# Kernel tuning notes

Hardware: AMD Instinct MI355X
Metric: run time of the kernel (lower is better)

The kernel has to match this reference:

```python
import jax, jax.numpy as jnp
import numpy as np

EPS_LN = 1e-5


def segment_softmax(logits, seg, num_segments):
    m = jax.ops.segment_max(logits, seg, num_segments=num_segments)
    e = jnp.exp(logits - m[seg])
    s = jax.ops.segment_sum(e, seg, num_segments=num_segments)
    return e / (s[seg] + 1e-16)


def transformer_conv(x, src, dst, edge_attr, Wq, bq, Wk, bk, Wv, bv, We, Ws, bs):
    # PyG TransformerConv, heads=1: key/value gathered at source, query at dst,
    # transformed edge feature added to both key and value (message).
    N, D = x.shape[0], Wq.shape[1]
    q = (x @ Wq + bq)[dst]                      # [E, D]
    e = edge_attr @ We                          # [E, D] (lin_edge, no bias)
    k = (x @ Wk + bk)[src] + e                  # [E, D]
    v = (x @ Wv + bv)[src] + e                  # [E, D]
    alpha = segment_softmax((q * k).sum(-1) / jnp.sqrt(jnp.float32(D)), dst, N)
    agg = jax.ops.segment_sum(alpha[:, None] * v, dst, num_segments=N)
    return agg + x @ Ws + bs                    # root_weight skip connection


def graph_layer_norm(x, w, b):
    # PyG LayerNorm mode='graph': normalize over all nodes AND features of the graph.
    mu = x.mean()
    xc = x - mu
    var = (xc * xc).mean()
    return xc * jax.lax.rsqrt(var + EPS_LN) * w + b


def setup_inputs():
    key = jax.random.key(0)
    ks = jax.random.split(key, 32)
    N, E, F_NODE, F_EDGE, H, D_OUT = 50000, 800000, 64, 16, 128, 1
    g = lambda k, shp, s=0.05: jax.random.normal(k, shp, jnp.float32) * s
    inp = {
        'x': jax.random.normal(ks[0], (N, F_NODE), jnp.float32),
        'edge_index': jax.random.randint(ks[1], (2, E), 0, N),
        'edge_attr': jax.random.normal(ks[2], (E, F_EDGE), jnp.float32),
        'fc1_w': g(ks[3], (F_NODE, H)), 'fc1_b': jnp.zeros((H,), jnp.float32),
        'c1_Wq': g(ks[4], (H, H)), 'c1_bq': jnp.zeros((H,), jnp.float32),
        'c1_Wk': g(ks[5], (H, H)), 'c1_bk': jnp.zeros((H,), jnp.float32),
        'c1_Wv': g(ks[6], (H, H)), 'c1_bv': jnp.zeros((H,), jnp.float32),
        'c1_We': g(ks[7], (F_EDGE, H)),
        'c1_Ws': g(ks[8], (H, H)), 'c1_bs': jnp.zeros((H,), jnp.float32),
        'ln1_w': jnp.ones((H,), jnp.float32), 'ln1_b': jnp.zeros((H,), jnp.float32),
        'c2_Wq': g(ks[9], (H, H)), 'c2_bq': jnp.zeros((H,), jnp.float32),
        'c2_Wk': g(ks[10], (H, H)), 'c2_bk': jnp.zeros((H,), jnp.float32),
        'c2_Wv': g(ks[11], (H, H)), 'c2_bv': jnp.zeros((H,), jnp.float32),
        'c2_We': g(ks[12], (F_EDGE, H)),
        'c2_Ws': g(ks[13], (H, H)), 'c2_bs': jnp.zeros((H,), jnp.float32),
        'ln2_w': jnp.ones((H,), jnp.float32), 'ln2_b': jnp.zeros((H,), jnp.float32),
        'fc2_w': g(ks[14], (H, D_OUT)), 'fc2_b': jnp.zeros((D_OUT,), jnp.float32),
    }
    return inp


def reference(x, edge_index, edge_attr,
              fc1_w, fc1_b,
              c1_Wq, c1_bq, c1_Wk, c1_bk, c1_Wv, c1_bv, c1_We, c1_Ws, c1_bs,
              ln1_w, ln1_b,
              c2_Wq, c2_bq, c2_Wk, c2_bk, c2_Wv, c2_bv, c2_We, c2_Ws, c2_bs,
              ln2_w, ln2_b,
              fc2_w, fc2_b):
    src, dst = edge_index[0], edge_index[1]
    hx = x @ fc1_w + fc1_b
    h = transformer_conv(hx, src, dst, edge_attr,
                         c1_Wq, c1_bq, c1_Wk, c1_bk, c1_Wv, c1_bv, c1_We, c1_Ws, c1_bs)
    h = jax.nn.relu(graph_layer_norm(h, ln1_w, ln1_b))
    h = transformer_conv(h, src, dst, edge_attr,
                         c2_Wq, c2_bq, c2_Wk, c2_bk, c2_Wv, c2_bv, c2_We, c2_Ws, c2_bs)
    h = jax.nn.relu(graph_layer_norm(h, ln2_w, ln2_b))
    return h @ fc2_w + fc2_b
```

## Files before the change

kernel.cpp:

```cpp
#include <hip/hip_runtime.h>
#include <math.h>

#define HH 128
#define FIN 64
#define FE 16
#define SCAN_CHUNK 512

__global__ __launch_bounds__(256) void zero_int4(int4* __restrict__ p, int n4) {
  const int stride = gridDim.x * 256;
  for (int i = blockIdx.x * 256 + threadIdx.x; i < n4; i += stride)
    p[i] = make_int4(0, 0, 0, 0);
}

__global__ __launch_bounds__(256) void hist_kernel(
    const int* __restrict__ dstArr, int* __restrict__ deg, int E) {
  const int e = blockIdx.x * 256 + threadIdx.x;
  if (e < E) atomicAdd(deg + dstArr[e], 1);
}

__global__ __launch_bounds__(256) void scan1(
    const int* __restrict__ deg, int* __restrict__ out, int* __restrict__ sums, int n) {
  __shared__ int lds[256];
  const int t = threadIdx.x;
  const int i0 = blockIdx.x * SCAN_CHUNK + t * 2;
  const int v0 = (i0 < n) ? deg[i0] : 0;
  const int v1 = (i0 + 1 < n) ? deg[i0 + 1] : 0;
  const int tsum = v0 + v1;
  lds[t] = tsum;
  __syncthreads();
  for (int off = 1; off < 256; off <<= 1) {
    const int x = (t >= off) ? lds[t - off] : 0;
    __syncthreads();
    lds[t] += x;
    __syncthreads();
  }
  const int excl = lds[t] - tsum;
  if (i0 < n) out[i0] = excl;
  if (i0 + 1 < n) out[i0 + 1] = excl + v0;
  if (t == 255) sums[blockIdx.x] = lds[255];
}

__global__ __launch_bounds__(256) void scan2(int* __restrict__ sums, int nb) {
  __shared__ int lds[256];
  const int t = threadIdx.x;
  const int v = (t < nb) ? sums[t] : 0;
  lds[t] = v;
  __syncthreads();
  for (int off = 1; off < 256; off <<= 1) {
    const int x = (t >= off) ? lds[t - off] : 0;
    __syncthreads();
    lds[t] += x;
    __syncthreads();
  }
  if (t < nb) sums[t] = lds[t] - v;
}

__global__ __launch_bounds__(256) void scan3(
    int* __restrict__ out, const int* __restrict__ sums, int n) {
  const int add = sums[blockIdx.x];
  const int i0 = blockIdx.x * SCAN_CHUNK + threadIdx.x * 2;
  if (i0 < n) out[i0] += add;
  if (i0 + 1 < n) out[i0 + 1] += add;
}

__global__ __launch_bounds__(256) void scatter_kernel(
    const int* __restrict__ dstArr, const int* __restrict__ off,
    int* __restrict__ cursor, int* __restrict__ eids, int E) {
  const int e = blockIdx.x * 256 + threadIdx.x;
  if (e < E) {
    const int d = dstArr[e];
    const int p = atomicAdd(cursor + d, 1);
    eids[off[d] + p] = e;
  }
}

template<int K, int RB>
__global__ __launch_bounds__(128) void gemm_rows(
    const float* __restrict__ in, const float* __restrict__ W,
    const float* __restrict__ bias, float* __restrict__ out, int nrows) {
  __shared__ float tile[RB * K];
  const int r0 = blockIdx.x * RB;
  const int tid = threadIdx.x;
  {
    const int rows = min(RB, nrows - r0);
    const int cnt = rows * K / 4;
    const float4* src = (const float4*)(in + (size_t)r0 * K);
    float4* dst = (float4*)tile;
    for (int i = tid; i < cnt; i += 128) dst[i] = src[i];
  }
  __syncthreads();
  const int j = tid;
  float acc[RB];
  const float bj = bias[j];
#pragma unroll
  for (int r = 0; r < RB; ++r) acc[r] = bj;
#pragma unroll 4
  for (int k = 0; k < K; ++k) {
    float w = W[k * HH + j];
#pragma unroll
    for (int r = 0; r < RB; ++r) acc[r] += tile[r * K + k] * w;
  }
#pragma unroll
  for (int r = 0; r < RB; ++r) {
    int row = r0 + r;
    if (row < nrows) out[(size_t)row * HH + j] = acc[r];
  }
}

template<int RB>
__global__ __launch_bounds__(128) void qkvs_kernel(
    float* __restrict__ x,
    const float* __restrict__ Wq, const float* __restrict__ bq,
    const float* __restrict__ Wk, const float* __restrict__ bk,
    const float* __restrict__ Wv, const float* __restrict__ bv,
    const float* __restrict__ Ws, const float* __restrict__ bs,
    float* __restrict__ q, float* __restrict__ k, float* __restrict__ v,
    int nrows) {
  __shared__ float tile[RB * HH];
  const int r0 = blockIdx.x * RB;
  const int tid = threadIdx.x;
  {
    const int rows = min(RB, nrows - r0);
    const int cnt = rows * HH / 4;
    const float4* src = (const float4*)(x + (size_t)r0 * HH);
    float4* dst = (float4*)tile;
    for (int i = tid; i < cnt; i += 128) dst[i] = src[i];
  }
  __syncthreads();
  const int j = tid;
  float aq[RB], ak[RB], av[RB], as_[RB];
  const float bqj = bq[j], bkj = bk[j], bvj = bv[j], bsj = bs[j];
#pragma unroll
  for (int r = 0; r < RB; ++r) { aq[r] = bqj; ak[r] = bkj; av[r] = bvj; as_[r] = bsj; }
#pragma unroll 2
  for (int kk = 0; kk < HH; ++kk) {
    const float wq = Wq[kk * HH + j];
    const float wk = Wk[kk * HH + j];
    const float wv = Wv[kk * HH + j];
    const float ws = Ws[kk * HH + j];
#pragma unroll
    for (int r = 0; r < RB; ++r) {
      const float xv = tile[r * HH + kk];
      aq[r] += xv * wq; ak[r] += xv * wk; av[r] += xv * wv; as_[r] += xv * ws;
    }
  }
#pragma unroll
  for (int r = 0; r < RB; ++r) {
    int row = r0 + r;
    if (row < nrows) {
      const size_t o = (size_t)row * HH + j;
      q[o] = aq[r]; k[o] = ak[r]; v[o] = av[r]; x[o] = as_[r];
    }
  }
}

__global__ __launch_bounds__(256) void dst_conv(
    const int* __restrict__ csr_off, const int* __restrict__ deg,
    const int* __restrict__ csr_eid, const int* __restrict__ srcArr,
    const float* __restrict__ ea, const float* __restrict__ We,
    const float* __restrict__ q, const float* __restrict__ k,
    const float* __restrict__ v, float* __restrict__ xio,
    double* __restrict__ partials, int N) {
  const int lane = threadIdx.x & 63;
  const int wv = (blockIdx.x * blockDim.x + threadIdx.x) >> 6;
  const int nw = (gridDim.x * blockDim.x) >> 6;
  const int f0 = lane * 2;
  float wec0[FE], wec1[FE];
#pragma unroll
  for (int i = 0; i < FE; ++i) {
    wec0[i] = We[i * HH + f0];
    wec1[i] = We[i * HH + f0 + 1];
  }
  const float rs = 0.088388347648318447f;
  float s = 0.f, sq = 0.f;
  for (int d = wv; d < N; d += nw) {
    const int du = __builtin_amdgcn_readfirstlane(d);
    const int off = csr_off[du];
    const int cnt = deg[du];
    const float2 qv = *(const float2*)(q + (size_t)du * HH + f0);
    float a0 = 0.f, a1 = 0.f, wsum = 0.f;
    int eid = (cnt > 0) ? __builtin_amdgcn_readfirstlane(csr_eid[off]) : 0;
    int sn  = (cnt > 0) ? __builtin_amdgcn_readfirstlane(srcArr[eid]) : 0;
    for (int i = 0; i < cnt; ++i) {
      const int eid_n = (i + 1 < cnt) ? __builtin_amdgcn_readfirstlane(csr_eid[off + i + 1]) : 0;
      const int sn_n  = (i + 1 < cnt) ? __builtin_amdgcn_readfirstlane(srcArr[eid_n]) : 0;
      const float4* eap4 = (const float4*)(ea + (size_t)eid * FE);
      const float4 e0 = eap4[0], e1 = eap4[1], e2 = eap4[2], e3 = eap4[3];
      float ep0, ep1;
      ep0 = e0.x * wec0[0] + e0.y * wec0[1] + e0.z * wec0[2] + e0.w * wec0[3]
          + e1.x * wec0[4] + e1.y * wec0[5] + e1.z * wec0[6] + e1.w * wec0[7]
          + e2.x * wec0[8] + e2.y * wec0[9] + e2.z * wec0[10] + e2.w * wec0[11]
          + e3.x * wec0[12] + e3.y * wec0[13] + e3.z * wec0[14] + e3.w * wec0[15];
      ep1 = e0.x * wec1[0] + e0.y * wec1[1] + e0.z * wec1[2] + e0.w * wec1[3]
          + e1.x * wec1[4] + e1.y * wec1[5] + e1.z * wec1[6] + e1.w * wec1[7]
          + e2.x * wec1[8] + e2.y * wec1[9] + e2.z * wec1[10] + e2.w * wec1[11]
          + e3.x * wec1[12] + e3.y * wec1[13] + e3.z * wec1[14] + e3.w * wec1[15];
      const float2 kv = *(const float2*)(k + (size_t)sn * HH + f0);
      const float2 vv = *(const float2*)(v + (size_t)sn * HH + f0);
      float part = qv.x * (kv.x + ep0) + qv.y * (kv.y + ep1);
#pragma unroll
      for (int o = 32; o; o >>= 1) part += __shfl_xor(part, o);
      const float w = __expf(part * rs);
      wsum += w;
      a0 += w * (vv.x + ep0);
      a1 += w * (vv.y + ep1);
      eid = eid_n;
      sn = sn_n;
    }
    const float inv = 1.0f / (wsum + 1e-16f);
    float* xr = xio + (size_t)du * HH + f0;
    const float o0 = fmaf(a0, inv, xr[0]);
    const float o1 = fmaf(a1, inv, xr[1]);
    xr[0] = o0;
    xr[1] = o1;
    s += o0 + o1;
    sq += o0 * o0 + o1 * o1;
  }
#pragma unroll
  for (int o = 32; o; o >>= 1) {
    s += __shfl_xor(s, o);
    sq += __shfl_xor(sq, o);
  }
  __shared__ double red[8];
  const int w = threadIdx.x >> 6;
  if ((threadIdx.x & 63) == 0) { red[w * 2] = (double)s; red[w * 2 + 1] = (double)sq; }
  __syncthreads();
  if (threadIdx.x == 0) {
    partials[(size_t)blockIdx.x * 2] = red[0] + red[2] + red[4] + red[6];
    partials[(size_t)blockIdx.x * 2 + 1] = red[1] + red[3] + red[5] + red[7];
  }
}

__global__ __launch_bounds__(256) void ln_reduce2(
    const double* __restrict__ partials, int nb, float* __restrict__ stats,
    double inv_count) {
  double s = 0.0, sq = 0.0;
  for (int i = threadIdx.x; i < nb; i += 256) {
    s += partials[(size_t)i * 2];
    sq += partials[(size_t)i * 2 + 1];
  }
#pragma unroll
  for (int off = 32; off; off >>= 1) {
    s += __shfl_xor(s, off);
    sq += __shfl_xor(sq, off);
  }
  __shared__ double red[8];
  const int w = threadIdx.x >> 6;
  if ((threadIdx.x & 63) == 0) { red[w * 2] = s; red[w * 2 + 1] = sq; }
  __syncthreads();
  if (threadIdx.x == 0) {
    double S = 0, SQ = 0;
    for (int i = 0; i < 4; ++i) { S += red[i * 2]; SQ += red[i * 2 + 1]; }
    const double mu = S * inv_count;
    const double var = SQ * inv_count - mu * mu;
    stats[0] = (float)mu;
    stats[1] = (float)(1.0 / sqrt(var + 1e-5));
  }
}

__global__ __launch_bounds__(256) void ln_apply(
    float* __restrict__ x, const float* __restrict__ stats,
    const float* __restrict__ w, const float* __restrict__ b, int total4) {
  const int i = blockIdx.x * 256 + threadIdx.x;
  if (i >= total4) return;
  const float mu = stats[0], rstd = stats[1];
  const float4 xv = ((const float4*)x)[i];
  const float4 wv = ((const float4*)w)[i & 31];
  const float4 bv = ((const float4*)b)[i & 31];
  float4 o;
  o.x = fmaxf(fmaf((xv.x - mu) * rstd, wv.x, bv.x), 0.f);
  o.y = fmaxf(fmaf((xv.y - mu) * rstd, wv.y, bv.y), 0.f);
  o.z = fmaxf(fmaf((xv.z - mu) * rstd, wv.z, bv.z), 0.f);
  o.w = fmaxf(fmaf((xv.w - mu) * rstd, wv.w, bv.w), 0.f);
  ((float4*)x)[i] = o;
}

__global__ __launch_bounds__(256) void fc2_kernel(
    const float* __restrict__ h, const float* __restrict__ w,
    const float* __restrict__ b, float* __restrict__ out, int n) {
  const int lane = threadIdx.x & 63;
  const int node = (blockIdx.x * blockDim.x + threadIdx.x) >> 6;
  if (node >= n) return;
  const float2 hv = *(const float2*)(h + (size_t)node * HH + lane * 2);
  const float2 wv = *(const float2*)(w + lane * 2);
  float p = hv.x * wv.x + hv.y * wv.y;
#pragma unroll
  for (int off = 32; off; off >>= 1) p += __shfl_xor(p, off);
  if (lane == 0) out[node] = p + b[0];
}

extern "C" void kernel_launch(void* const* d_in, const int* in_sizes, int n_in,
                              void* d_out, int out_size, void* d_ws, size_t ws_size,
                              hipStream_t stream) {
  const float* x      = (const float*)d_in[0];
  const int*   eidx   = (const int*)d_in[1];
  const float* ea     = (const float*)d_in[2];
  const float* fc1_w  = (const float*)d_in[3];
  const float* fc1_b  = (const float*)d_in[4];
  const float* c1_Wq  = (const float*)d_in[5];
  const float* c1_bq  = (const float*)d_in[6];
  const float* c1_Wk  = (const float*)d_in[7];
  const float* c1_bk  = (const float*)d_in[8];
  const float* c1_Wv  = (const float*)d_in[9];
  const float* c1_bv  = (const float*)d_in[10];
  const float* c1_We  = (const float*)d_in[11];
  const float* c1_Ws  = (const float*)d_in[12];
  const float* c1_bs  = (const float*)d_in[13];
  const float* ln1_w  = (const float*)d_in[14];
  const float* ln1_b  = (const float*)d_in[15];
  const float* c2_Wq  = (const float*)d_in[16];
  const float* c2_bq  = (const float*)d_in[17];
  const float* c2_Wk  = (const float*)d_in[18];
  const float* c2_bk  = (const float*)d_in[19];
  const float* c2_Wv  = (const float*)d_in[20];
  const float* c2_bv  = (const float*)d_in[21];
  const float* c2_We  = (const float*)d_in[22];
  const float* c2_Ws  = (const float*)d_in[23];
  const float* c2_bs  = (const float*)d_in[24];
  const float* ln2_w  = (const float*)d_in[25];
  const float* ln2_b  = (const float*)d_in[26];
  const float* fc2_w  = (const float*)d_in[27];
  const float* fc2_b  = (const float*)d_in[28];

  const int N = in_sizes[0] / FIN;
  const int E = in_sizes[2] / FE;
  const int* srcA = eidx;
  const int* dstA = eidx + E;

  float* ws    = (float*)d_ws;
  const size_t NH = (size_t)N * HH;
  float* bufX  = ws;
  float* qb    = ws + NH;
  float* kb    = ws + 2 * NH;
  float* vb    = ws + 3 * NH;
  int* ibase   = (int*)(ws + 4 * NH);
  int* deg     = ibase;
  int* cursor  = ibase + N;
  int* csr_off = ibase + 2 * N;
  int* csr_eid = ibase + 3 * N;
  size_t icnt  = ((size_t)3 * N + E + 3) & ~(size_t)3;
  double* partials = (double*)(ibase + icnt);
  const int NB = 2048;
  float* stats = (float*)(partials + 2 * NB);
  int* sums    = (int*)(stats + 4);

  const int total4 = (int)(NH / 4);
  const int gRows  = (N + 15) / 16;
  const int gE     = (E + 255) / 256;
  const int nb1    = (N + SCAN_CHUNK - 1) / SCAN_CHUNK;
  const double invC = 1.0 / (double)NH;

  zero_int4<<<128, 256, 0, stream>>>((int4*)deg, (2 * N + 3) / 4);
  hist_kernel<<<gE, 256, 0, stream>>>(dstA, deg, E);
  scan1<<<nb1, 256, 0, stream>>>(deg, csr_off, sums, N);
  scan2<<<1, 256, 0, stream>>>(sums, nb1);
  scan3<<<nb1, 256, 0, stream>>>(csr_off, sums, N);
  scatter_kernel<<<gE, 256, 0, stream>>>(dstA, csr_off, cursor, csr_eid, E);

  gemm_rows<FIN, 16><<<gRows, 128, 0, stream>>>(x, fc1_w, fc1_b, bufX, N);
  qkvs_kernel<16><<<gRows, 128, 0, stream>>>(bufX, c1_Wq, c1_bq, c1_Wk, c1_bk,
                                             c1_Wv, c1_bv, c1_Ws, c1_bs,
                                             qb, kb, vb, N);
  dst_conv<<<NB, 256, 0, stream>>>(csr_off, deg, csr_eid, srcA, ea, c1_We,
                                   qb, kb, vb, bufX, partials, N);
  ln_reduce2<<<1, 256, 0, stream>>>(partials, NB, stats, invC);
  ln_apply<<<(total4 + 255) / 256, 256, 0, stream>>>(bufX, stats, ln1_w, ln1_b, total4);

  qkvs_kernel<16><<<gRows, 128, 0, stream>>>(bufX, c2_Wq, c2_bq, c2_Wk, c2_bk,
                                             c2_Wv, c2_bv, c2_Ws, c2_bs,
                                             qb, kb, vb, N);
  dst_conv<<<NB, 256, 0, stream>>>(csr_off, deg, csr_eid, srcA, ea, c2_We,
                                   qb, kb, vb, bufX, partials, N);
  ln_reduce2<<<1, 256, 0, stream>>>(partials, NB, stats, invC);
  ln_apply<<<(total4 + 255) / 256, 256, 0, stream>>>(bufX, stats, ln2_w, ln2_b, total4);

  fc2_kernel<<<(N + 3) / 4, 256, 0, stream>>>(bufX, fc2_w, fc2_b, (float*)d_out, N);
}
```

Before: 979.0 us.

## Factor edge projection out of per-edge loop and process nodes with 16-lane groups

Uses linearity to avoid projecting edge features to 128 dims per edge. A new kernel precomputes q·We^T (16 values per node), so the score only needs a 16-wide dot with the raw edge attributes. The weighted sum of edge attributes is accumulated per node and multiplied by We once at the end. Each destination node is now handled by a 16-lane group with float4 loads instead of a full wavefront, which cuts per-edge FLOPs and widens memory accesses. This adds a small extra kernel and workspace buffer, and trades lane parallelism per node for more nodes in flight, which may increase divergence on skewed degree distributions.

```diff
diff --git a/kernel.cpp b/kernel.cpp
--- a/kernel.cpp
+++ b/kernel.cpp
@@ -154,67 +154,109 @@
   }
 }
 
-__global__ __launch_bounds__(256) void dst_conv(
+__global__ __launch_bounds__(128) void qe_kernel(
+    const float* __restrict__ q, const float* __restrict__ We,
+    float* __restrict__ qe, int N) {
+  __shared__ float qs[8 * HH];
+  __shared__ float WeT[HH * 17];
+  const int tid = threadIdx.x;
+  for (int u = tid; u < FE * HH; u += 128) {
+    const int i = u >> 7, j = u & 127;
+    WeT[j * 17 + i] = We[u];
+  }
+  const int r0 = blockIdx.x * 8;
+  const int rows = min(8, N - r0);
+  const int cnt4 = rows * (HH / 4);
+  const float4* src = (const float4*)(q + (size_t)r0 * HH);
+  for (int u = tid; u < cnt4; u += 128) ((float4*)qs)[u] = src[u];
+  __syncthreads();
+  const int r = tid >> 4, i = tid & 15;
+  if (r < rows) {
+    const float* qrow = qs + r * HH;
+    float acc = 0.f;
+#pragma unroll 8
+    for (int j = 0; j < HH; ++j) acc += qrow[j] * WeT[j * 17 + i];
+    qe[(size_t)(r0 + r) * FE + i] = acc;
+  }
+}
+
+__global__ __launch_bounds__(256) void dst_conv16(
     const int* __restrict__ csr_off, const int* __restrict__ deg,
     const int* __restrict__ csr_eid, const int* __restrict__ srcArr,
     const float* __restrict__ ea, const float* __restrict__ We,
-    const float* __restrict__ q, const float* __restrict__ k,
-    const float* __restrict__ v, float* __restrict__ xio,
-    double* __restrict__ partials, int N) {
+    const float* __restrict__ q, const float* __restrict__ qe,
+    const float* __restrict__ k, const float* __restrict__ v,
+    float* __restrict__ xio, double* __restrict__ partials, int N) {
+  __shared__ float WeS[FE * HH];
+  for (int u = threadIdx.x; u < FE * HH; u += 256) WeS[u] = We[u];
+  __syncthreads();
   const int lane = threadIdx.x & 63;
-  const int wv = (blockIdx.x * blockDim.x + threadIdx.x) >> 6;
-  const int nw = (gridDim.x * blockDim.x) >> 6;
-  const int f0 = lane * 2;
-  float wec0[FE], wec1[FE];
-#pragma unroll
-  for (int i = 0; i < FE; ++i) {
-    wec0[i] = We[i * HH + f0];
-    wec1[i] = We[i * HH + f0 + 1];
-  }
+  const int gl = lane & 15;
+  const int gbase = lane & 48;
+  const int grp = (blockIdx.x * 256 + threadIdx.x) >> 4;
+  const int ngrp = (gridDim.x * 256) >> 4;
   const float rs = 0.088388347648318447f;
   float s = 0.f, sq = 0.f;
-  for (int d = wv; d < N; d += nw) {
-    const int du = __builtin_amdgcn_readfirstlane(d);
-    const int off = csr_off[du];
-    const int cnt = deg[du];
-    const float2 qv = *(const float2*)(q + (size_t)du * HH + f0);
-    float a0 = 0.f, a1 = 0.f, wsum = 0.f;
-    int eid = (cnt > 0) ? __builtin_amdgcn_readfirstlane(csr_eid[off]) : 0;
-    int sn  = (cnt > 0) ? __builtin_amdgcn_readfirstlane(srcArr[eid]) : 0;
+  for (int d = grp; d < N; d += ngrp) {
+    const int off = csr_off[d];
+    const int cnt = deg[d];
+    const float4* qp = (const float4*)(q + (size_t)d * HH);
+    const float4 qc0 = qp[gl], qc1 = qp[16 + gl];
+    const float qel = qe[(size_t)d * FE + gl];
+    float4 a0 = {0.f, 0.f, 0.f, 0.f}, a1 = {0.f, 0.f, 0.f, 0.f};
+    float wsum = 0.f, t = 0.f;
+    int eid = (cnt > 0) ? csr_eid[off] : 0;
+    int sn = (cnt > 0) ? srcArr[eid] : 0;
     for (int i = 0; i < cnt; ++i) {
-      const int eid_n = (i + 1 < cnt) ? __builtin_amdgcn_readfirstlane(csr_eid[off + i + 1]) : 0;
-      const int sn_n  = (i + 1 < cnt) ? __builtin_amdgcn_readfirstlane(srcArr[eid_n]) : 0;
-      const float4* eap4 = (const float4*)(ea + (size_t)eid * FE);
-      const float4 e0 = eap4[0], e1 = eap4[1], e2 = eap4[2], e3 = eap4[3];
-      float ep0, ep1;
-      ep0 = e0.x * wec0[0] + e0.y * wec0[1] + e0.z * wec0[2] + e0.w * wec0[3]
-          + e1.x * wec0[4] + e1.y * wec0[5] + e1.z * wec0[6] + e1.w * wec0[7]
-          + e2.x * wec0[8] + e2.y * wec0[9] + e2.z * wec0[10] + e2.w * wec0[11]
-          + e3.x * wec0[12] + e3.y * wec0[13] + e3.z * wec0[14] + e3.w * wec0[15];
-      ep1 = e0.x * wec1[0] + e0.y * wec1[1] + e0.z * wec1[2] + e0.w * wec1[3]
-          + e1.x * wec1[4] + e1.y * wec1[5] + e1.z * wec1[6] + e1.w * wec1[7]
-          + e2.x * wec1[8] + e2.y * wec1[9] + e2.z * wec1[10] + e2.w * wec1[11]
-          + e3.x * wec1[12] + e3.y * wec1[13] + e3.z * wec1[14] + e3.w * wec1[15];
-      const float2 kv = *(const float2*)(k + (size_t)sn * HH + f0);
-      const float2 vv = *(const float2*)(v + (size_t)sn * HH + f0);
-      float part = qv.x * (kv.x + ep0) + qv.y * (kv.y + ep1);
-#pragma unroll
-      for (int o = 32; o; o >>= 1) part += __shfl_xor(part, o);
+      const bool nxt = (i + 1 < cnt);
+      const int eid_n = nxt ? csr_eid[off + i + 1] : 0;
+      const int sn_n = nxt ? srcArr[eid_n] : 0;
+      const float eal = ea[(size_t)eid * FE + gl];
+      const float4* kp = (const float4*)(k + (size_t)sn * HH);
+      const float4* vp = (const float4*)(v + (size_t)sn * HH);
+      const float4 kc0 = kp[gl], kc1 = kp[16 + gl];
+      const float4 vc0 = vp[gl], vc1 = vp[16 + gl];
+      float part = qc0.x * kc0.x + qc0.y * kc0.y + qc0.z * kc0.z + qc0.w * kc0.w
+                 + qc1.x * kc1.x + qc1.y * kc1.y + qc1.z * kc1.z + qc1.w * kc1.w
+                 + qel * eal;
+      part += __shfl_xor(part, 1);
+      part += __shfl_xor(part, 2);
+      part += __shfl_xor(part, 4);
+      part += __shfl_xor(part, 8);
       const float w = __expf(part * rs);
       wsum += w;
-      a0 += w * (vv.x + ep0);
-      a1 += w * (vv.y + ep1);
+      a0.x += w * vc0.x; a0.y += w * vc0.y; a0.z += w * vc0.z; a0.w += w * vc0.w;
+      a1.x += w * vc1.x; a1.y += w * vc1.y; a1.z += w * vc1.z; a1.w += w * vc1.w;
+      t += w * eal;
       eid = eid_n;
       sn = sn_n;
     }
+    float4 c0 = {0.f, 0.f, 0.f, 0.f}, c1 = {0.f, 0.f, 0.f, 0.f};
+#pragma unroll
+    for (int i = 0; i < FE; ++i) {
+      const float ti = __shfl(t, gbase + i);
+      const float4 w0 = *(const float4*)(WeS + i * HH + gl * 4);
+      const float4 w1 = *(const float4*)(WeS + i * HH + 64 + gl * 4);
+      c0.x += ti * w0.x; c0.y += ti * w0.y; c0.z += ti * w0.z; c0.w += ti * w0.w;
+      c1.x += ti * w1.x; c1.y += ti * w1.y; c1.z += ti * w1.z; c1.w += ti * w1.w;
+    }
     const float inv = 1.0f / (wsum + 1e-16f);
-    float* xr = xio + (size_t)du * HH + f0;
-    const float o0 = fmaf(a0, inv, xr[0]);
-    const float o1 = fmaf(a1, inv, xr[1]);
-    xr[0] = o0;
-    xr[1] = o1;
-    s += o0 + o1;
-    sq += o0 * o0 + o1 * o1;
+    float4* xr = (float4*)(xio + (size_t)d * HH);
+    const float4 sk0 = xr[gl], sk1 = xr[16 + gl];
+    float4 o0, o1;
+    o0.x = fmaf(a0.x + c0.x, inv, sk0.x);
+    o0.y = fmaf(a0.y + c0.y, inv, sk0.y);
+    o0.z = fmaf(a0.z + c0.z, inv, sk0.z);
+    o0.w = fmaf(a0.w + c0.w, inv, sk0.w);
+    o1.x = fmaf(a1.x + c1.x, inv, sk1.x);
+    o1.y = fmaf(a1.y + c1.y, inv, sk1.y);
+    o1.z = fmaf(a1.z + c1.z, inv, sk1.z);
+    o1.w = fmaf(a1.w + c1.w, inv, sk1.w);
+    xr[gl] = o0;
+    xr[16 + gl] = o1;
+    s += o0.x + o0.y + o0.z + o0.w + o1.x + o1.y + o1.z + o1.w;
+    sq += o0.x * o0.x + o0.y * o0.y + o0.z * o0.z + o0.w * o0.w
+        + o1.x * o1.x + o1.y * o1.y + o1.z * o1.z + o1.w * o1.w;
   }
 #pragma unroll
   for (int o = 32; o; o >>= 1) {
@@ -339,7 +381,8 @@
   int* csr_off = ibase + 2 * N;
   int* csr_eid = ibase + 3 * N;
   size_t icnt  = ((size_t)3 * N + E + 3) & ~(size_t)3;
-  double* partials = (double*)(ibase + icnt);
+  float* qeb   = (float*)(ibase + icnt);
+  double* partials = (double*)(qeb + (size_t)N * FE);
   const int NB = 2048;
   float* stats = (float*)(partials + 2 * NB);
   int* sums    = (int*)(stats + 4);
@@ -348,6 +391,7 @@
   const int gRows  = (N + 15) / 16;
   const int gE     = (E + 255) / 256;
   const int nb1    = (N + SCAN_CHUNK - 1) / SCAN_CHUNK;
+  const int gQe    = (N + 7) / 8;
   const double invC = 1.0 / (double)NH;
 
   zero_int4<<<128, 256, 0, stream>>>((int4*)deg, (2 * N + 3) / 4);
@@ -361,16 +405,18 @@
   qkvs_kernel<16><<<gRows, 128, 0, stream>>>(bufX, c1_Wq, c1_bq, c1_Wk, c1_bk,
                                              c1_Wv, c1_bv, c1_Ws, c1_bs,
                                              qb, kb, vb, N);
-  dst_conv<<<NB, 256, 0, stream>>>(csr_off, deg, csr_eid, srcA, ea, c1_We,
-                                   qb, kb, vb, bufX, partials, N);
+  qe_kernel<<<gQe, 128, 0, stream>>>(qb, c1_We, qeb, N);
+  dst_conv16<<<NB, 256, 0, stream>>>(csr_off, deg, csr_eid, srcA, ea, c1_We,
+                                     qb, qeb, kb, vb, bufX, partials, N);
   ln_reduce2<<<1, 256, 0, stream>>>(partials, NB, stats, invC);
   ln_apply<<<(total4 + 255) / 256, 256, 0, stream>>>(bufX, stats, ln1_w, ln1_b, total4);
 
   qkvs_kernel<16><<<gRows, 128, 0, stream>>>(bufX, c2_Wq, c2_bq, c2_Wk, c2_bk,
                                              c2_Wv, c2_bv, c2_Ws, c2_bs,
                                              qb, kb, vb, N);
-  dst_conv<<<NB, 256, 0, stream>>>(csr_off, deg, csr_eid, srcA, ea, c2_We,
-                                   qb, kb, vb, bufX, partials, N);
+  qe_kernel<<<gQe, 128, 0, stream>>>(qb, c2_We, qeb, N);
+  dst_conv16<<<NB, 256, 0, stream>>>(csr_off, deg, csr_eid, srcA, ea, c2_We,
+                                     qb, qeb, kb, vb, bufX, partials, N);
   ln_reduce2<<<1, 256, 0, stream>>>(partials, NB, stats, invC);
   ln_apply<<<(total4 + 255) / 256, 256, 0, stream>>>(bufX, stats, ln2_w, ln2_b, total4);
 
```

Result: faster. 937.0 us (-4.3%).
